# Performance work log

Hardware: AMD Instinct MI355X
Metric: run time of the kernel (lower is better)

The kernel has to match this reference:

```python
import jax, jax.numpy as jnp
import numpy as np
from jax import lax

B, C, H, W = 16, 256, 32, 32
HK, WK = 16, 16
NH = 8              # num_heads
HD = C // NH        # head_dim = 32
N = H * W           # 1024
M = HK * WK         # 256
EXP = 3             # attn_expansion
HID = NH * EXP      # 24 hidden channels in DLA
EPS = 1e-5


def setup_inputs() -> dict:
    key = jax.random.key(0)
    ks = jax.random.split(key, 16)
    s = 0.02
    return {
        "q": jax.random.normal(ks[0], (B, C, H, W), jnp.float32),
        "kv": jax.random.normal(ks[1], (B, C, HK, WK), jnp.float32),
        "Wq": jax.random.normal(ks[2], (C, C), jnp.float32) * s,
        "Wkv": jax.random.normal(ks[3], (2 * C, C), jnp.float32) * s,
        "Wp": jax.random.normal(ks[4], (C, C), jnp.float32) * s,
        "bp": jnp.zeros((C,), jnp.float32),
        "rpb": jnp.ones((N, M), jnp.float32),
        "W_exp": jax.random.normal(ks[5], (HID, NH), jnp.float32) * s,   # 1x1 conv heads->hidden
        "g1": jnp.ones((HID,), jnp.float32),
        "b1": jnp.zeros((HID,), jnp.float32),
        "W_dw": jax.random.normal(ks[6], (HID, 1, 3, 3), jnp.float32) * s,  # depthwise 3x3
        "g2": jnp.ones((HID,), jnp.float32),
        "b2": jnp.zeros((HID,), jnp.float32),
        "W_red": jax.random.normal(ks[7], (NH, HID), jnp.float32) * s,  # 1x1 conv hidden->heads
        "g3": jnp.ones((NH,), jnp.float32),
        "b3": jnp.zeros((NH,), jnp.float32),
    }


def group_norm(x, gamma, beta, groups):
    b, c, h, w = x.shape
    xg = x.reshape(b, groups, c // groups, h, w)
    mu = xg.mean(axis=(2, 3, 4), keepdims=True)
    var = xg.var(axis=(2, 3, 4), keepdims=True)
    xn = ((xg - mu) * lax.rsqrt(var + EPS)).reshape(b, c, h, w)
    return xn * gamma[None, :, None, None] + beta[None, :, None, None]


def swish(x):
    return x * jax.nn.sigmoid(x)


def dla(a, W_exp, g1, b1, W_dw, g2, b2, W_red, g3, b3):
    # a: [B, NH, N, M] treated as NCHW image with C=num_heads
    x = jnp.einsum('bcnm,oc->bonm', a, W_exp)              # 1x1 expand -> [B,HID,N,M]
    x = swish(group_norm(x, g1, b1, EXP))
    x = lax.conv_general_dilated(
        x, W_dw, window_strides=(1, 1), padding='SAME',
        feature_group_count=HID,
        dimension_numbers=('NCHW', 'OIHW', 'NCHW'))        # depthwise 3x3
    x = swish(group_norm(x, g2, b2, EXP))
    x = jnp.einsum('bcnm,oc->bonm', x, W_red)              # 1x1 reduce -> [B,NH,N,M]
    x = group_norm(x, g3, b3, 1)                            # no activation
    return x


def reference(q, kv, Wq, Wkv, Wp, bp, rpb, W_exp, g1, b1, W_dw, g2, b2, W_red, g3, b3):
    b = q.shape[0]
    scale = HD ** -0.5
    # kv path: [B,C,HK,WK] -> [B,M,C] -> Linear(C->2C)
    kv_t = kv.reshape(b, C, M).transpose(0, 2, 1)
    kvp = kv_t @ Wkv.T                                     # [B,M,2C]
    kvp = kvp.reshape(b, M, 2, NH, HD).transpose(2, 0, 3, 1, 4)  # [2,B,NH,M,HD]
    k, v = kvp[0], kvp[1]
    # q path: [B,C,H,W] -> [B,N,C] -> Linear -> [B,NH,N,HD]
    qf = (q.reshape(b, C, N).transpose(0, 2, 1) @ Wq.T)
    qh = qf.reshape(b, N, NH, HD).transpose(0, 2, 1, 3)
    attn = jnp.einsum('bhnd,bhmd->bhnm', qh, k) * scale + rpb[None, None]
    attn = jax.nn.softmax(attn, axis=-1)
    attn = dla(attn, W_exp, g1, b1, W_dw, g2, b2, W_red, g3, b3)
    out = jnp.einsum('bhnm,bhmd->bhnd', attn, v)           # [B,NH,N,HD]
    out = out.transpose(0, 2, 1, 3).reshape(b, N, C)
    out = out @ Wp.T + bp
    return out.transpose(0, 2, 1).reshape(b, C, H, W)
```

## Files before the change

kernel.cpp:

```cpp
#include <hip/hip_runtime.h>
#include <math.h>

#define Bb 16
#define Cc 256
#define Nn 1024
#define Mm 256
#define NHh 8
#define HDd 32
#define HIDh 24
#define NMs (Nn*Mm)
#define TTB 8
#define CHUNK 8
#define EPSf 1e-5f
#define SCALEf 0.17677669529663687f
#define STP 32

typedef float v2f __attribute__((ext_vector_type(2)));
typedef __attribute__((ext_vector_type(8))) short bf8v;
typedef __attribute__((ext_vector_type(4))) float f4v;

__device__ __forceinline__ float wave_sum(float v){
#pragma unroll
  for (int off=32; off; off>>=1) v += __shfl_xor(v, off, 64);
  return v;
}
__device__ __forceinline__ float sigm_(float x){ return __builtin_amdgcn_rcpf(1.f + __expf(-x)); }
__device__ __forceinline__ float swish_(float x){ return x * sigm_(x); }
__device__ __forceinline__ v2f swish2(v2f x){
  v2f r;
  r.x = x.x * sigm_(x.x);
  r.y = x.y * sigm_(x.y);
  return r;
}
__device__ __forceinline__ unsigned short f2bf(float f){
  unsigned u = __float_as_uint(f);
  u += 0x7fffu + ((u >> 16) & 1u);
  return (unsigned short)(u >> 16);
}
__device__ __forceinline__ unsigned cvtpk(float lo, float hi){
  unsigned r;
  asm("v_cvt_pk_bf16_f32 %0, %1, %2" : "=v"(r) : "v"(lo), "v"(hi));
  return r;
}
__device__ __forceinline__ float bfup(unsigned short s){ return __uint_as_float(((unsigned)s) << 16); }
__device__ __forceinline__ float bflo(unsigned u){ return __uint_as_float(u << 16); }
__device__ __forceinline__ float bfhi(unsigned u){ return __uint_as_float(u & 0xffff0000u); }
__device__ __forceinline__ void gload_lds16(const void* g, void* l){
  __builtin_amdgcn_global_load_lds(
      (const __attribute__((address_space(1))) unsigned int*)g,
      (__attribute__((address_space(3))) unsigned int*)l, 16, 0, 0);
}

template<int HASBIAS>
__launch_bounds__(256)
__global__ void gemm_mfma(const float* __restrict__ A,
                          const float* __restrict__ W,
                          const float* __restrict__ bias,
                          float* __restrict__ O)
{
  __shared__ __align__(16) unsigned short Wt[64 * 40];
  __shared__ __align__(16) unsigned short At[64 * 40];
  const int b = blockIdx.z;
  const int i0 = blockIdx.x * 64;
  const int j0 = blockIdx.y * 64;
  const int tid = threadIdx.x;
  const int lane = tid & 63, wv = tid >> 6;
  const int wj = (wv >> 1) * 32, wi = (wv & 1) * 32;
  const int l15 = lane & 15, l4 = lane >> 4;

  const float* Ab = A + (long)b * Cc * Nn;
  const int sj = tid >> 2, skh = (tid & 3) * 8;
  const int si = tid & 63, skb = (tid >> 6) * 8;

  f4v acc[2][2] = {};
  for (int k0 = 0; k0 < Cc; k0 += 32) {
    float wreg[8];
    {
      const float* wp = W + (long)(j0 + sj) * Cc + k0 + skh;
      *(f4v*)&wreg[0] = *(const f4v*)&wp[0];
      *(f4v*)&wreg[4] = *(const f4v*)&wp[4];
    }
    float areg[8];
    {
      const float* ap = Ab + (long)(k0 + skb) * Nn + i0 + si;
#pragma unroll
      for (int e = 0; e < 8; e++) areg[e] = ap[(long)e * Nn];
    }
    __syncthreads();
    {
      unsigned pk[4];
#pragma unroll
      for (int t = 0; t < 4; t++) pk[t] = cvtpk(wreg[2*t], wreg[2*t+1]);
      *(uint4*)&Wt[sj*40 + skh] = make_uint4(pk[0], pk[1], pk[2], pk[3]);
#pragma unroll
      for (int t = 0; t < 4; t++) pk[t] = cvtpk(areg[2*t], areg[2*t+1]);
      *(uint4*)&At[si*40 + skb] = make_uint4(pk[0], pk[1], pk[2], pk[3]);
    }
    __syncthreads();
    bf8v af[2], bf[2];
#pragma unroll
    for (int fm = 0; fm < 2; fm++)
      af[fm] = *(const bf8v*)&Wt[(wj + fm*16 + l15)*40 + l4*8];
#pragma unroll
    for (int fn = 0; fn < 2; fn++)
      bf[fn] = *(const bf8v*)&At[(wi + fn*16 + l15)*40 + l4*8];
#pragma unroll
    for (int fm = 0; fm < 2; fm++)
#pragma unroll
      for (int fn = 0; fn < 2; fn++)
        acc[fm][fn] = __builtin_amdgcn_mfma_f32_16x16x32_bf16(af[fm], bf[fn], acc[fm][fn], 0, 0, 0);
  }
#pragma unroll
  for (int fm = 0; fm < 2; fm++) {
    f4v bv = {0.f, 0.f, 0.f, 0.f};
    if (HASBIAS) bv = *(const f4v*)&bias[j0 + wj + fm*16 + l4*4];
#pragma unroll
    for (int fn = 0; fn < 2; fn++) {
      const int jj = j0 + wj + fm*16 + l4*4;
      const int ii = i0 + wi + fn*16 + l15;
      float* op = O + ((long)b * Cc + jj) * Nn + ii;
#pragma unroll
      for (int r = 0; r < 4; r++)
        op[(long)r * Nn] = acc[fm][fn][r] + bv[r];
    }
  }
}

template<int MODE>
__launch_bounds__(256)
__global__ void gemm_tn(const float* __restrict__ A, const float* __restrict__ W,
                        const float* __restrict__ bias, float* __restrict__ O1,
                        float* __restrict__ O2, int Kdim, long sAb, int sAk, int sAi)
{
  __shared__ __align__(16) float As[16][68];
  __shared__ __align__(16) float Ws[16][68];
  const int b  = blockIdx.z;
  const int i0 = blockIdx.x * 64;
  const int j0 = blockIdx.y * 64;
  const int tid = threadIdx.x;
  const int tx = tid & 15, ty = tid >> 4;
  const float* Ab = A + (long)b * sAb;
  float acc[4][4] = {};
  for (int k0 = 0; k0 < Kdim; k0 += 16) {
#pragma unroll
    for (int t = 0; t < 4; t++) {
      int idx = tid + t * 256;
      int kk, ii;
      if (sAi == 1) { kk = idx >> 6; ii = idx & 63; }
      else          { ii = idx >> 4; kk = idx & 15; }
      As[kk][ii] = Ab[(long)(k0 + kk) * sAk + (long)(i0 + ii) * sAi];
    }
#pragma unroll
    for (int t = 0; t < 4; t++) {
      int idx = tid + t * 256;
      int jj = idx & 63, kk = idx >> 6;
      Ws[kk][jj] = W[(long)(j0 + jj) * Kdim + (k0 + kk)];
    }
    __syncthreads();
#pragma unroll
    for (int kk = 0; kk < 16; kk++) {
      const float4 av = *(const float4*)&As[kk][tx * 4];
      const float4 wv = *(const float4*)&Ws[kk][ty * 4];
      const float a4[4] = {av.x, av.y, av.z, av.w};
      const float w4[4] = {wv.x, wv.y, wv.z, wv.w};
#pragma unroll
      for (int u = 0; u < 4; u++)
#pragma unroll
        for (int v = 0; v < 4; v++)
          acc[u][v] = fmaf(a4[u], w4[v], acc[u][v]);
    }
    __syncthreads();
  }
#pragma unroll
  for (int v = 0; v < 4; v++) {
    const int j = j0 + ty * 4 + v;
    const int two = j >> 8, jj = j & 255;
    const int h = jj >> 5, d = jj & 31;
    float* p = two ? O2 : O1;
#pragma unroll
    for (int u = 0; u < 4; u++)
      p[(((long)b * NHh + h) * Mm + (i0 + tx * 4 + u)) * HDd + d] = acc[u][v];
  }
}

__launch_bounds__(256)
__global__ void compute_sv(const float* __restrict__ vb, float* __restrict__ sv)
{
  __shared__ float red[256];
  const int bh = blockIdx.x, tid = threadIdx.x;
  const int d = tid & 31, ch = tid >> 5;
  const float* vp = vb + (long)bh * Mm * HDd;
  float s = 0.f;
  for (int m = ch; m < Mm; m += 8) s += vp[m * HDd + d];
  red[tid] = s;
  __syncthreads();
  if (tid < 32) {
    float t = 0.f;
#pragma unroll
    for (int cc = 0; cc < 8; cc++) t += red[cc * 32 + tid];
    sv[(long)bh * HDd + tid] = t;
  }
}

__launch_bounds__(256)
__global__ void attn_softmax(const float* __restrict__ qhT, const float* __restrict__ kb,
                             const float* __restrict__ rpb, unsigned short* __restrict__ attn)
{
  __shared__ __align__(16) unsigned short Kt[Mm * 40];
  __shared__ __align__(16) unsigned short Qt[64 * 40];
  const int b = blockIdx.z, h = blockIdx.y, n0 = blockIdx.x * 64;
  const int tid = threadIdx.x;
  const int lane = tid & 63, wv = tid >> 6;
  const int l15 = lane & 15, l4 = lane >> 4;
  {
    const float* kp = kb + ((long)b * NHh + h) * Mm * HDd;
#pragma unroll
    for (int u = 0; u < 8; u++) {
      const int f = tid + u * 256;
      const int m = f >> 3, dq = (f & 7) * 4;
      const f4v k4 = *(const f4v*)&kp[m * HDd + dq];
      *(uint2*)&Kt[m * 40 + dq] = make_uint2(cvtpk(k4.x, k4.y), cvtpk(k4.z, k4.w));
    }
  }
  {
    const float* qp = qhT + ((long)b * NHh + h) * HDd * Nn + n0;
#pragma unroll
    for (int u = 0; u < 4; u++) {
      const int f = tid + u * 256;
      const int n = f & 63, d2 = (f >> 6) * 2;
      const float q0 = qp[(long)d2 * Nn + n];
      const float q1 = qp[(long)(d2 + 1) * Nn + n];
      *(unsigned*)&Qt[n * 40 + d2] = cvtpk(q0, q1);
    }
  }
  __syncthreads();
  const bf8v qf = *(const bf8v*)&Qt[(wv * 16 + l15) * 40 + l4 * 8];
  f4v S[16];
#pragma unroll
  for (int mt = 0; mt < 16; mt++) {
    const bf8v kf = *(const bf8v*)&Kt[(mt * 16 + l15) * 40 + l4 * 8];
    f4v z = {0.f, 0.f, 0.f, 0.f};
    S[mt] = __builtin_amdgcn_mfma_f32_16x16x32_bf16(kf, qf, z, 0, 0, 0);
  }
  const int n = n0 + wv * 16 + l15;
  const float* rp = rpb + (long)n * Mm;
  float mx = -1e30f;
#pragma unroll
  for (int mt = 0; mt < 16; mt++) {
    const f4v r4 = *(const f4v*)&rp[mt * 16 + l4 * 4];
    S[mt][0] = fmaf(S[mt][0], SCALEf, r4.x);
    S[mt][1] = fmaf(S[mt][1], SCALEf, r4.y);
    S[mt][2] = fmaf(S[mt][2], SCALEf, r4.z);
    S[mt][3] = fmaf(S[mt][3], SCALEf, r4.w);
    mx = fmaxf(mx, fmaxf(fmaxf(S[mt][0], S[mt][1]), fmaxf(S[mt][2], S[mt][3])));
  }
  mx = fmaxf(mx, __shfl_xor(mx, 16, 64));
  mx = fmaxf(mx, __shfl_xor(mx, 32, 64));
  float sum = 0.f;
#pragma unroll
  for (int mt = 0; mt < 16; mt++) {
    S[mt][0] = __expf(S[mt][0] - mx);
    S[mt][1] = __expf(S[mt][1] - mx);
    S[mt][2] = __expf(S[mt][2] - mx);
    S[mt][3] = __expf(S[mt][3] - mx);
    sum += (S[mt][0] + S[mt][1]) + (S[mt][2] + S[mt][3]);
  }
  sum += __shfl_xor(sum, 16, 64);
  sum += __shfl_xor(sum, 32, 64);
  const float inv = __builtin_amdgcn_rcpf(sum);
  unsigned short* ap = attn + (((long)b * NHh + h) * Nn + n) * Mm;
#pragma unroll
  for (int mt = 0; mt < 16; mt++) {
    const unsigned p0 = cvtpk(S[mt][0] * inv, S[mt][1] * inv);
    const unsigned p1 = cvtpk(S[mt][2] * inv, S[mt][3] * inv);
    *(uint2*)&ap[mt * 16 + l4 * 4] = make_uint2(p0, p1);
  }
}

__launch_bounds__(256)
__global__ void gram_stats(const unsigned short* __restrict__ attn, float* __restrict__ G)
{
  __shared__ float red[36][4];
  const int b = blockIdx.y, tid = threadIdx.x;
  const unsigned short* ap = attn + (long)b * NHh * NMs + (long)blockIdx.x * 2048 + tid * 8;
  float a[8][8];
#pragma unroll
  for (int h = 0; h < 8; h++) {
    const uint4 v = *(const uint4*)&ap[(long)h * NMs];
    a[h][0] = bflo(v.x); a[h][1] = bfhi(v.x); a[h][2] = bflo(v.y); a[h][3] = bfhi(v.y);
    a[h][4] = bflo(v.z); a[h][5] = bfhi(v.z); a[h][6] = bflo(v.w); a[h][7] = bfhi(v.w);
  }
  float g[36];
  int t = 0;
#pragma unroll
  for (int i = 0; i < 8; i++)
#pragma unroll
    for (int j = i; j < 8; j++, t++) {
      float s = 0.f;
#pragma unroll
      for (int m = 0; m < 8; m++) s = fmaf(a[i][m], a[j][m], s);
      g[t] = s;
    }
  const int lane = tid & 63, wid = tid >> 6;
#pragma unroll
  for (int t2 = 0; t2 < 36; t2++) {
    const float s = wave_sum(g[t2]);
    if (lane == 0) red[t2][wid] = s;
  }
  __syncthreads();
  if (tid < 36)
    atomicAdd(&G[((long)b * 36 + tid) * STP],
              red[tid][0] + red[tid][1] + red[tid][2] + red[tid][3]);
}

__launch_bounds__(768, 6)
__global__ void dla_pass_b(const unsigned short* __restrict__ attn,
                           const float* __restrict__ Wexp,
                           const float* __restrict__ g1, const float* __restrict__ b1,
                           const float* __restrict__ G, const float* __restrict__ Wdw,
                           unsigned short* __restrict__ x2, float* __restrict__ stats2c, int b0)
{
  __shared__ __align__(16) unsigned short sl[(TTB + 2) * NHh * Mm];
  const int tid = threadIdx.x;
  const int wv = tid >> 6, lane = tid & 63;
  const int bc = blockIdx.y, b = b0 + bc;
  const int n0 = blockIdx.x * TTB;
  const int c0 = wv * 2;
  const int g = wv >> 2;

  {
    const unsigned short* abase = attn + (long)b * NHh * NMs;
    const int q_lo = lane >> 5;
    const int m0 = (lane & 31) * 8;
#pragma unroll
    for (int i = 0; i < 4; i++) {
      const int pr = wv + i * 12;
      if (pr < 40) {
        const int pp = pr * 2;
        const int row = pp >> 3;
        const int nn = n0 - 1 + row;
        if (nn >= 0 && nn < Nn) {
          const int h = (pp + q_lo) & 7;
          gload_lds16(abase + (long)h * NMs + (long)nn * Mm + m0, &sl[pp * Mm]);
        }
      }
    }
  }

  float mu, rs;
  {
    const float* Gb = G + (long)b * 36 * STP;
    float sum = 0.f, sumsq = 0.f;
    for (int c = g * 8; c < g * 8 + 8; c++) {
      float w[8];
#pragma unroll
      for (int h = 0; h < 8; h++) w[h] = Wexp[c * 8 + h];
      float wsu = 0.f;
#pragma unroll
      for (int h = 0; h < 8; h++) wsu += w[h];
      sum += wsu;
      float s2 = 0.f;
      int t = 0;
#pragma unroll
      for (int i = 0; i < 8; i++)
#pragma unroll
        for (int j = i; j < 8; j++, t++) {
          const float f = (i == j) ? 1.f : 2.f;
          s2 = fmaf(f * w[i] * w[j], Gb[t * STP], s2);
        }
      sumsq += s2;
    }
    const float cnt = 8.f * NMs;
    mu = sum * ((float)Nn / cnt);
    const float var = sumsq / cnt - mu * mu;
    rs = rsqrtf(var + EPSf);
  }
  v2f we2[8], wd2[9], B12;
  {
    const float A10 = rs * g1[c0], A11 = rs * g1[c0 + 1];
    B12.x = b1[c0] - mu * A10;
    B12.y = b1[c0 + 1] - mu * A11;
#pragma unroll
    for (int h = 0; h < NHh; h++) {
      we2[h].x = Wexp[c0 * NHh + h] * A10;
      we2[h].y = Wexp[(c0 + 1) * NHh + h] * A11;
    }
#pragma unroll
    for (int k = 0; k < 9; k++) {
      wd2[k].x = Wdw[c0 * 9 + k];
      wd2[k].y = Wdw[(c0 + 1) * 9 + k];
    }
  }
  __syncthreads();

  v2f s1p[4] = {}, s2p[4] = {};
  v2f smp = {0.f, 0.f}, sqp = {0.f, 0.f};
  for (int r = -1; r <= TTB; r++) {
    const int nn = n0 + r;
    const bool rowv = (nn >= 0 && nn < Nn);
    v2f xp[4];
    if (rowv) {
#pragma unroll
      for (int mi = 0; mi < 4; mi++) xp[mi] = B12;
      const unsigned short* sp = &sl[(r + 1) * NHh * Mm + lane * 4];
#pragma unroll
      for (int h = 0; h < NHh; h++) {
        const ushort4 v = *(const ushort4*)&sp[h * Mm];
        xp[0] += we2[h] * bfup(v.x);
        xp[1] += we2[h] * bfup(v.y);
        xp[2] += we2[h] * bfup(v.z);
        xp[3] += we2[h] * bfup(v.w);
      }
#pragma unroll
      for (int mi = 0; mi < 4; mi++) xp[mi] = swish2(xp[mi]);
    } else {
#pragma unroll
      for (int mi = 0; mi < 4; mi++) xp[mi] = (v2f){0.f, 0.f};
    }
    v2f xl, xr;
    xl.x = __shfl_up(xp[3].x, 1);  xl.y = __shfl_up(xp[3].y, 1);
    xr.x = __shfl_down(xp[0].x, 1); xr.y = __shfl_down(xp[0].y, 1);
    if (lane == 0)  { xl = (v2f){0.f, 0.f}; }
    if (lane == 63) { xr = (v2f){0.f, 0.f}; }
    const v2f L[4] = {xl, xp[0], xp[1], xp[2]};
    const v2f R[4] = {xp[1], xp[2], xp[3], xr};
    v2f y[4];
#pragma unroll
    for (int mi = 0; mi < 4; mi++) {
      const v2f u0 = wd2[0] * L[mi] + wd2[1] * xp[mi] + wd2[2] * R[mi];
      const v2f u1 = wd2[3] * L[mi] + wd2[4] * xp[mi] + wd2[5] * R[mi];
      const v2f u2 = wd2[6] * L[mi] + wd2[7] * xp[mi] + wd2[8] * R[mi];
      y[mi] = s2p[mi] + u2;
      s2p[mi] = s1p[mi] + u1;
      s1p[mi] = u0;
    }
    if (r >= 1) {
#pragma unroll
      for (int mi = 0; mi < 4; mi++) {
        smp += y[mi];
        sqp += y[mi] * y[mi];
      }
      const int nw = n0 + r - 1;
      const unsigned w0 = cvtpk(y[0].x, y[1].x), w1 = cvtpk(y[2].x, y[3].x);
      const unsigned w2 = cvtpk(y[0].y, y[1].y), w3 = cvtpk(y[2].y, y[3].y);
      unsigned short* xq = x2 + ((long)(bc * Nn + nw) * HIDh + c0) * Mm + lane * 4;
      *(uint2*)xq        = make_uint2(w0, w1);
      *(uint2*)(xq + Mm) = make_uint2(w2, w3);
    }
  }
  {
    const float vs0 = wave_sum(smp.x), vq0 = wave_sum(sqp.x);
    const float vs1 = wave_sum(smp.y), vq1 = wave_sum(sqp.y);
    if (lane == 0) {
      atomicAdd(&stats2c[((long)b * HIDh + c0) * STP], vs0);
      atomicAdd(&stats2c[((long)b * HIDh + c0) * STP + 1], vq0);
      atomicAdd(&stats2c[((long)b * HIDh + c0 + 1) * STP], vs1);
      atomicAdd(&stats2c[((long)b * HIDh + c0 + 1) * STP + 1], vq1);
    }
  }
}

__launch_bounds__(256)
__global__ void dla_pass_c(const unsigned short* __restrict__ x2, const float* __restrict__ g2,
                           const float* __restrict__ b2, const float* __restrict__ stats2c,
                           const float* __restrict__ Wred, unsigned short* __restrict__ a2,
                           float* __restrict__ partial3, int b0)
{
  __shared__ float wA[HIDh], wB[HIDh], wrs[HIDh][NHh];
  __shared__ float red2[2][4];
  const int tid = threadIdx.x;
  const int wv = tid >> 6, lane = tid & 63;
  const int bc = blockIdx.y, b = b0 + bc;
  if (tid < HIDh) {
    const int c = tid, g = c >> 3;
    float s = 0.f, q = 0.f;
#pragma unroll
    for (int cc = 0; cc < 8; cc++) {
      s += stats2c[((long)b * HIDh + g * 8 + cc) * STP];
      q += stats2c[((long)b * HIDh + g * 8 + cc) * STP + 1];
    }
    const float cnt = 8.f * NMs;
    const float mu = s / cnt;
    const float var = q / cnt - mu * mu;
    const float A2 = rsqrtf(var + EPSf) * g2[c];
    wA[c] = A2; wB[c] = b2[c] - mu * A2;
  }
  if (tid < HIDh * NHh) {
    const int c = tid >> 3, h = tid & 7;
    wrs[c][h] = Wred[h * HIDh + c];
  }
  __syncthreads();
  const int rsel = lane >> 5, ms = lane & 31;
  const int n = blockIdx.x * 8 + wv * 2 + rsel;
  const unsigned short* xp = x2 + (long)(bc * Nn + n) * HIDh * Mm + ms * 8;
  float red[NHh][8] = {};
#pragma unroll
  for (int c = 0; c < HIDh; c++) {
    const uint4 xv = *(const uint4*)&xp[c * Mm];
    const float Ac = wA[c], Bc = wB[c];
    float sw[8];
    sw[0] = swish_(fmaf(bflo(xv.x), Ac, Bc));
    sw[1] = swish_(fmaf(bfhi(xv.x), Ac, Bc));
    sw[2] = swish_(fmaf(bflo(xv.y), Ac, Bc));
    sw[3] = swish_(fmaf(bfhi(xv.y), Ac, Bc));
    sw[4] = swish_(fmaf(bflo(xv.z), Ac, Bc));
    sw[5] = swish_(fmaf(bfhi(xv.z), Ac, Bc));
    sw[6] = swish_(fmaf(bflo(xv.w), Ac, Bc));
    sw[7] = swish_(fmaf(bfhi(xv.w), Ac, Bc));
#pragma unroll
    for (int h = 0; h < NHh; h++) {
      const float w = wrs[c][h];
#pragma unroll
      for (int mi = 0; mi < 8; mi++) red[h][mi] = fmaf(w, sw[mi], red[h][mi]);
    }
  }
  float s3 = 0.f, q3 = 0.f;
#pragma unroll
  for (int h = 0; h < NHh; h++) {
    uint4 st;
    st.x = cvtpk(red[h][0], red[h][1]);
    st.y = cvtpk(red[h][2], red[h][3]);
    st.z = cvtpk(red[h][4], red[h][5]);
    st.w = cvtpk(red[h][6], red[h][7]);
    *(uint4*)&a2[(((long)b * NHh + h) * Nn + n) * Mm + ms * 8] = st;
#pragma unroll
    for (int mi = 0; mi < 8; mi++) {
      s3 += red[h][mi]; q3 = fmaf(red[h][mi], red[h][mi], q3);
    }
  }
  s3 = wave_sum(s3); q3 = wave_sum(q3);
  if (lane == 0) { red2[0][wv] = s3; red2[1][wv] = q3; }
  __syncthreads();
  if (tid < 2) {
    float t = red2[tid][0] + red2[tid][1] + red2[tid][2] + red2[tid][3];
    partial3[((long)b * 128 + blockIdx.x) * 2 + tid] = t;
  }
}

__launch_bounds__(128)
__global__ void finalize_stats3(const float* __restrict__ partial3, float* __restrict__ stats3)
{
  __shared__ float red2[2][2];
  const int b = blockIdx.x, tid = threadIdx.x;
  const int lane = tid & 63, wv = tid >> 6;
  float s = partial3[((long)b * 128 + tid) * 2];
  float q = partial3[((long)b * 128 + tid) * 2 + 1];
  s = wave_sum(s); q = wave_sum(q);
  if (lane == 0) { red2[0][wv] = s; red2[1][wv] = q; }
  __syncthreads();
  if (tid < 2)
    stats3[b * 2 + tid] = red2[tid][0] + red2[tid][1];
}

__launch_bounds__(256)
__global__ void pv_mfma(const unsigned short* __restrict__ a2, const float* __restrict__ vb,
                        const float* __restrict__ sv, const float* __restrict__ stats3,
                        const float* __restrict__ g3, const float* __restrict__ b3,
                        float* __restrict__ o)
{
  __shared__ __align__(16) unsigned short Vt[32 * 264];
  const int b = blockIdx.z, h = blockIdx.y, n0 = blockIdx.x * 128;
  const int tid = threadIdx.x;
  const int lane = tid & 63, wv = tid >> 6;
  const int l15 = lane & 15, l4 = lane >> 4;
  {
    const float* vp = vb + ((long)b * NHh + h) * Mm * HDd;
#pragma unroll
    for (int u = 0; u < 32; u++) {
      const int idx = tid + u * 256;
      const int m = idx >> 5, d = idx & 31;
      Vt[d * 264 + m] = f2bf(vp[idx]);
    }
  }
  __syncthreads();
  const unsigned short* ap = a2 + (((long)b * NHh + h) * Nn + n0) * Mm;
  f4v acc[2][2] = {};
#pragma unroll 2
  for (int k0 = 0; k0 < Mm; k0 += 32) {
    bf8v af[2], bf[2];
#pragma unroll
    for (int fm = 0; fm < 2; fm++)
      af[fm] = *(const bf8v*)&Vt[(fm * 16 + l15) * 264 + k0 + l4 * 8];
#pragma unroll
    for (int fn = 0; fn < 2; fn++)
      bf[fn] = *(const bf8v*)&ap[(long)(wv * 32 + fn * 16 + l15) * Mm + k0 + l4 * 8];
#pragma unroll
    for (int fm = 0; fm < 2; fm++)
#pragma unroll
      for (int fn = 0; fn < 2; fn++)
        acc[fm][fn] = __builtin_amdgcn_mfma_f32_16x16x32_bf16(af[fm], bf[fn], acc[fm][fn], 0, 0, 0);
  }
  const float cnt = (float)(NHh * NMs);
  const float mu = stats3[b * 2] / cnt;
  const float var = stats3[b * 2 + 1] / cnt - mu * mu;
  const float r3 = rsqrtf(var + EPSf);
  const float alpha = r3 * g3[h];
  const float beta = b3[h] - mu * alpha;
#pragma unroll
  for (int fm = 0; fm < 2; fm++) {
#pragma unroll
    for (int r = 0; r < 4; r++) {
      const int d = fm * 16 + l4 * 4 + r;
      const float bv = beta * sv[((long)b * NHh + h) * HDd + d];
      float* op = o + ((long)b * Cc + h * HDd + d) * Nn + n0 + wv * 32 + l15;
#pragma unroll
      for (int fn = 0; fn < 2; fn++)
        op[fn * 16] = fmaf(alpha, acc[fm][fn][r], bv);
    }
  }
}

extern "C" void kernel_launch(void* const* d_in, const int* in_sizes, int n_in,
                              void* d_out, int out_size, void* d_ws, size_t ws_size,
                              hipStream_t stream) {
  const float* q    = (const float*)d_in[0];
  const float* kv   = (const float*)d_in[1];
  const float* Wq   = (const float*)d_in[2];
  const float* Wkv  = (const float*)d_in[3];
  const float* Wp   = (const float*)d_in[4];
  const float* bp   = (const float*)d_in[5];
  const float* rpb  = (const float*)d_in[6];
  const float* Wexp = (const float*)d_in[7];
  const float* g1   = (const float*)d_in[8];
  const float* b1   = (const float*)d_in[9];
  const float* Wdw  = (const float*)d_in[10];
  const float* g2   = (const float*)d_in[11];
  const float* b2   = (const float*)d_in[12];
  const float* Wred = (const float*)d_in[13];
  const float* g3   = (const float*)d_in[14];
  const float* b3   = (const float*)d_in[15];
  float* out = (float*)d_out;

  float* ws = (float*)d_ws;
  size_t off = 0;
  auto alloc = [&](size_t n) { float* p = ws + off; off += n; return p; };
  float* attnf   = alloc((size_t)Bb * NHh * NMs / 2);
  float* a2f     = alloc((size_t)Bb * NHh * NMs / 2);
  float* big     = alloc((size_t)CHUNK * HIDh * NMs / 2);
  float* kbuf    = alloc((size_t)Bb * NHh * Mm * HDd);
  float* vbuf    = alloc((size_t)Bb * NHh * Mm * HDd);
  float* sv      = alloc((size_t)Bb * NHh * HDd);
  float* G       = alloc((size_t)Bb * 36 * STP);
  float* stats2c = alloc((size_t)Bb * HIDh * STP);
  float* stats3  = alloc(Bb * 2);
  float* partial3= alloc((size_t)Bb * 128 * 2);
  unsigned short* attn = (unsigned short*)attnf;
  unsigned short* a2 = (unsigned short*)a2f;
  float* qhT = big;
  unsigned short* x2 = (unsigned short*)big;
  float* oT = big;

  hipMemsetAsync(G, 0, (size_t)(Bb * 36 * STP + Bb * HIDh * STP) * sizeof(float), stream);

  gemm_mfma<0><<<dim3(Nn / 64, Cc / 64, Bb), 256, 0, stream>>>(q, Wq, nullptr, qhT);
  gemm_tn<1><<<dim3(Mm / 64, 512 / 64, Bb), 256, 0, stream>>>(
      kv, Wkv, nullptr, kbuf, vbuf, Cc, (long)Cc * Mm, Mm, 1);
  compute_sv<<<dim3(Bb * NHh), 256, 0, stream>>>(vbuf, sv);
  attn_softmax<<<dim3(Nn / 64, NHh, Bb), 256, 0, stream>>>(qhT, kbuf, rpb, attn);
  gram_stats<<<dim3(NMs / 2048, Bb), 256, 0, stream>>>(attn, G);

  for (int b0 = 0; b0 < Bb; b0 += CHUNK) {
    dla_pass_b<<<dim3(Nn / TTB, CHUNK), 768, 0, stream>>>(
        attn, Wexp, g1, b1, G, Wdw, x2, stats2c, b0);
    dla_pass_c<<<dim3(Nn / 8, CHUNK), 256, 0, stream>>>(
        x2, g2, b2, stats2c, Wred, a2, partial3, b0);
  }
  finalize_stats3<<<dim3(Bb), 128, 0, stream>>>(partial3, stats3);

  pv_mfma<<<dim3(Nn / 128, NHh, Bb), 256, 0, stream>>>(a2, vbuf, sv, stats3, g3, b3, oT);
  gemm_mfma<1><<<dim3(Nn / 64, Cc / 64, Bb), 256, 0, stream>>>(oT, Wp, bp, out);
}
```

Measured before the change: 433.5 us.

## Use bf16 MFMA GEMM for kv projection and double DLA row tile

The scalar fp32 kv projection GEMM is replaced by the bf16 MFMA GEMM, which now takes a runtime inner size and a scatter-to-head output mode. Separately, the DLA pass-B row tile grows from 8 to 16 rows, with the halo load loop rewritten for the larger LDS tile. Larger tiles cut redundant halo reads and launch count but raise LDS use per block and may lower occupancy. The bf16 kv projection lowers precision for k and v.

```diff
diff --git a/kernel.cpp b/kernel.cpp
--- a/kernel.cpp
+++ b/kernel.cpp
@@ -9,7 +9,7 @@
 #define HDd 32
 #define HIDh 24
 #define NMs (Nn*Mm)
-#define TTB 8
+#define TTB 16
 #define CHUNK 8
 #define EPSf 1e-5f
 #define SCALEf 0.17677669529663687f
@@ -51,12 +51,12 @@
       (__attribute__((address_space(3))) unsigned int*)l, 16, 0, 0);
 }
 
-template<int HASBIAS>
+template<int MODE>
 __launch_bounds__(256)
 __global__ void gemm_mfma(const float* __restrict__ A,
                           const float* __restrict__ W,
                           const float* __restrict__ bias,
-                          float* __restrict__ O)
+                          float* __restrict__ O1, float* __restrict__ O2, int Isize)
 {
   __shared__ __align__(16) unsigned short Wt[64 * 40];
   __shared__ __align__(16) unsigned short At[64 * 40];
@@ -68,7 +68,7 @@
   const int wj = (wv >> 1) * 32, wi = (wv & 1) * 32;
   const int l15 = lane & 15, l4 = lane >> 4;
 
-  const float* Ab = A + (long)b * Cc * Nn;
+  const float* Ab = A + (long)b * Cc * Isize;
   const int sj = tid >> 2, skh = (tid & 3) * 8;
   const int si = tid & 63, skb = (tid >> 6) * 8;
 
@@ -82,9 +82,9 @@
     }
     float areg[8];
     {
-      const float* ap = Ab + (long)(k0 + skb) * Nn + i0 + si;
-#pragma unroll
-      for (int e = 0; e < 8; e++) areg[e] = ap[(long)e * Nn];
+      const float* ap = Ab + (long)(k0 + skb) * Isize + i0 + si;
+#pragma unroll
+      for (int e = 0; e < 8; e++) areg[e] = ap[(long)e * Isize];
     }
     __syncthreads();
     {
@@ -112,74 +112,25 @@
   }
 #pragma unroll
   for (int fm = 0; fm < 2; fm++) {
+    const int jb = j0 + wj + fm*16 + l4*4;
     f4v bv = {0.f, 0.f, 0.f, 0.f};
-    if (HASBIAS) bv = *(const f4v*)&bias[j0 + wj + fm*16 + l4*4];
+    if (MODE == 2) bv = *(const f4v*)&bias[jb];
 #pragma unroll
     for (int fn = 0; fn < 2; fn++) {
-      const int jj = j0 + wj + fm*16 + l4*4;
       const int ii = i0 + wi + fn*16 + l15;
-      float* op = O + ((long)b * Cc + jj) * Nn + ii;
-#pragma unroll
-      for (int r = 0; r < 4; r++)
-        op[(long)r * Nn] = acc[fm][fn][r] + bv[r];
-    }
-  }
-}
-
-template<int MODE>
-__launch_bounds__(256)
-__global__ void gemm_tn(const float* __restrict__ A, const float* __restrict__ W,
-                        const float* __restrict__ bias, float* __restrict__ O1,
-                        float* __restrict__ O2, int Kdim, long sAb, int sAk, int sAi)
-{
-  __shared__ __align__(16) float As[16][68];
-  __shared__ __align__(16) float Ws[16][68];
-  const int b  = blockIdx.z;
-  const int i0 = blockIdx.x * 64;
-  const int j0 = blockIdx.y * 64;
-  const int tid = threadIdx.x;
-  const int tx = tid & 15, ty = tid >> 4;
-  const float* Ab = A + (long)b * sAb;
-  float acc[4][4] = {};
-  for (int k0 = 0; k0 < Kdim; k0 += 16) {
-#pragma unroll
-    for (int t = 0; t < 4; t++) {
-      int idx = tid + t * 256;
-      int kk, ii;
-      if (sAi == 1) { kk = idx >> 6; ii = idx & 63; }
-      else          { ii = idx >> 4; kk = idx & 15; }
-      As[kk][ii] = Ab[(long)(k0 + kk) * sAk + (long)(i0 + ii) * sAi];
-    }
-#pragma unroll
-    for (int t = 0; t < 4; t++) {
-      int idx = tid + t * 256;
-      int jj = idx & 63, kk = idx >> 6;
-      Ws[kk][jj] = W[(long)(j0 + jj) * Kdim + (k0 + kk)];
-    }
-    __syncthreads();
-#pragma unroll
-    for (int kk = 0; kk < 16; kk++) {
-      const float4 av = *(const float4*)&As[kk][tx * 4];
-      const float4 wv = *(const float4*)&Ws[kk][ty * 4];
-      const float a4[4] = {av.x, av.y, av.z, av.w};
-      const float w4[4] = {wv.x, wv.y, wv.z, wv.w};
-#pragma unroll
-      for (int u = 0; u < 4; u++)
-#pragma unroll
-        for (int v = 0; v < 4; v++)
-          acc[u][v] = fmaf(a4[u], w4[v], acc[u][v]);
-    }
-    __syncthreads();
-  }
-#pragma unroll
-  for (int v = 0; v < 4; v++) {
-    const int j = j0 + ty * 4 + v;
-    const int two = j >> 8, jj = j & 255;
-    const int h = jj >> 5, d = jj & 31;
-    float* p = two ? O2 : O1;
-#pragma unroll
-    for (int u = 0; u < 4; u++)
-      p[(((long)b * NHh + h) * Mm + (i0 + tx * 4 + u)) * HDd + d] = acc[u][v];
+      if (MODE == 1) {
+        const int two = jb >> 8, jj = jb & 255;
+        const int h = jj >> 5, d0 = jj & 31;
+        float* p = (two ? O2 : O1) + (((long)b * NHh + h) * Mm + ii) * HDd + d0;
+#pragma unroll
+        for (int r = 0; r < 4; r++) p[r] = acc[fm][fn][r];
+      } else {
+        float* op = O1 + ((long)b * Cc + jb) * (long)Isize + ii;
+#pragma unroll
+        for (int r = 0; r < 4; r++)
+          op[(long)r * Isize] = acc[fm][fn][r] + bv[r];
+      }
+    }
   }
 }
 
@@ -333,16 +284,13 @@
     const int q_lo = lane >> 5;
     const int m0 = (lane & 31) * 8;
 #pragma unroll
-    for (int i = 0; i < 4; i++) {
-      const int pr = wv + i * 12;
-      if (pr < 40) {
-        const int pp = pr * 2;
-        const int row = pp >> 3;
-        const int nn = n0 - 1 + row;
-        if (nn >= 0 && nn < Nn) {
-          const int h = (pp + q_lo) & 7;
-          gload_lds16(abase + (long)h * NMs + (long)nn * Mm + m0, &sl[pp * Mm]);
-        }
+    for (int i = 0; i < 6; i++) {
+      const int pp = (wv * 6 + i) * 2;
+      const int row = pp >> 3;
+      const int nn = n0 - 1 + row;
+      if (nn >= 0 && nn < Nn) {
+        const int h = (pp + q_lo) & 7;
+        gload_lds16(abase + (long)h * NMs + (long)nn * Mm + m0, &sl[pp * Mm]);
       }
     }
   }
@@ -652,9 +600,8 @@
 
   hipMemsetAsync(G, 0, (size_t)(Bb * 36 * STP + Bb * HIDh * STP) * sizeof(float), stream);
 
-  gemm_mfma<0><<<dim3(Nn / 64, Cc / 64, Bb), 256, 0, stream>>>(q, Wq, nullptr, qhT);
-  gemm_tn<1><<<dim3(Mm / 64, 512 / 64, Bb), 256, 0, stream>>>(
-      kv, Wkv, nullptr, kbuf, vbuf, Cc, (long)Cc * Mm, Mm, 1);
+  gemm_mfma<0><<<dim3(Nn / 64, Cc / 64, Bb), 256, 0, stream>>>(q, Wq, nullptr, qhT, nullptr, Nn);
+  gemm_mfma<1><<<dim3(Mm / 64, 512 / 64, Bb), 256, 0, stream>>>(kv, Wkv, nullptr, kbuf, vbuf, Mm);
   compute_sv<<<dim3(Bb * NHh), 256, 0, stream>>>(vbuf, sv);
   attn_softmax<<<dim3(Nn / 64, NHh, Bb), 256, 0, stream>>>(qhT, kbuf, rpb, attn);
   gram_stats<<<dim3(NMs / 2048, Bb), 256, 0, stream>>>(attn, G);
@@ -668,5 +615,5 @@
   finalize_stats3<<<dim3(Bb), 128, 0, stream>>>(partial3, stats3);
 
   pv_mfma<<<dim3(Nn / 128, NHh, Bb), 256, 0, stream>>>(a2, vbuf, sv, stats3, g3, b3, oT);
-  gemm_mfma<1><<<dim3(Nn / 64, Cc / 64, Bb), 256, 0, stream>>>(oT, Wp, bp, out);
-}
+  gemm_mfma<2><<<dim3(Nn / 64, Cc / 64, Bb), 256, 0, stream>>>(oT, Wp, bp, out, nullptr, Nn);
+}
```

Measured after the change: 394.2 us. 1.1x faster.
